# Kernel tuning notes

Hardware: AMD Instinct MI355X
Metric: run time of the kernel (lower is better)

Reference implementation:

```python
import jax, jax.numpy as jnp
import numpy as np

B, T, D_MODEL, N_HEADS = 2, 2048, 1024, 16


def setup_inputs() -> dict:
    key = jax.random.key(0)
    ks = jax.random.split(key, 5)
    w_scale = 0.02
    return {
        "x": jax.random.normal(ks[0], (B, T, D_MODEL), jnp.float32),
        "Wq": jax.random.normal(ks[1], (D_MODEL, D_MODEL), jnp.float32) * w_scale,
        "Wk": jax.random.normal(ks[2], (D_MODEL, D_MODEL), jnp.float32) * w_scale,
        "Wv": jax.random.normal(ks[3], (D_MODEL, D_MODEL), jnp.float32) * w_scale,
        "Wo": jax.random.normal(ks[4], (D_MODEL, D_MODEL), jnp.float32) * w_scale,
    }


def reference(x, Wq, Wk, Wv, Wo):
    Bv, Tv, _ = x.shape
    H = N_HEADS
    D = D_MODEL // H
    # Projections (torch nn.Linear: y = x @ W.T), split heads -> (B, H, T, D)
    q = (x @ Wq.T).reshape(Bv, Tv, H, D).transpose(0, 2, 1, 3)
    k = (x @ Wk.T).reshape(Bv, Tv, H, D).transpose(0, 2, 1, 3)
    v = (x @ Wv.T).reshape(Bv, Tv, H, D).transpose(0, 2, 1, 3)

    scale = jnp.sqrt(jnp.asarray(D, jnp.float32))
    scores = jnp.einsum("bhqd,bhkd->bhqk", q, k) / scale  # (B, H, T, T)

    # ALiBi bias: -|i-j| * slope_h, future positions masked to -inf (causal)
    slopes = jnp.asarray(
        [2.0 ** (-8.0 * h / H) for h in range(1, H + 1)], jnp.float32
    )
    pos = jnp.arange(Tv)
    dist = jnp.abs(pos[None, :] - pos[:, None]).astype(jnp.float32)  # (T, T)
    bias = -dist[None, :, :] * slopes[:, None, None]                 # (H, T, T)
    causal_mask = jnp.triu(jnp.ones((Tv, Tv), dtype=bool), 1)
    bias = jnp.where(causal_mask[None, :, :], -jnp.inf, bias)
    scores = scores + bias[None]  # (B, H, T, T)

    attn = jax.nn.softmax(scores, axis=-1)
    out = jnp.einsum("bhqk,bhkd->bhqd", attn, v)
    out = out.transpose(0, 2, 1, 3).reshape(Bv, Tv, D_MODEL)
    return out @ Wo.T
```

## Files before the change

kernel.cpp:

```cpp
#include <hip/hip_runtime.h>


#define DEV __device__ __forceinline__

typedef __attribute__((ext_vector_type(8))) short short8;
typedef __attribute__((ext_vector_type(4))) float f32x4;
typedef __attribute__((ext_vector_type(4))) unsigned short ushort4v;

DEV unsigned short f2bf(float f) {
  unsigned u = __builtin_bit_cast(unsigned, f);
  u += 0x7fffu + ((u >> 16) & 1u);
  return (unsigned short)(u >> 16);
}
DEV float bf2f(unsigned short u) {
  unsigned x = ((unsigned)u) << 16;
  return __builtin_bit_cast(float, x);
}

DEV void gl2lds16(const void* g, void* l) {
  __builtin_amdgcn_global_load_lds(
      (const __attribute__((address_space(1))) void*)g,
      (__attribute__((address_space(3))) void*)l, 16, 0, 0);
}

__global__ __launch_bounds__(256) void cvt_all(
    const float* __restrict__ x, const float* __restrict__ wq,
    const float* __restrict__ wk, const float* __restrict__ wv,
    const float* __restrict__ wo, unsigned short* __restrict__ xb,
    unsigned short* __restrict__ wqb, unsigned short* __restrict__ wkb,
    unsigned short* __restrict__ wvb, unsigned short* __restrict__ wob) {
  int b = blockIdx.x;
  const float* s;
  unsigned short* d;
  int off;
  if (b < 4096)      { s = x;  d = xb;  off = b; }
  else if (b < 5120) { s = wq; d = wqb; off = b - 4096; }
  else if (b < 6144) { s = wk; d = wkb; off = b - 5120; }
  else if (b < 7168) { s = wv; d = wvb; off = b - 6144; }
  else               { s = wo; d = wob; off = b - 7168; }
  int i = (off * 256 + threadIdx.x) * 4;
  float4 v = *(const float4*)(s + i);
  ushort4v o = {f2bf(v.x), f2bf(v.y), f2bf(v.z), f2bf(v.w)};
  *(ushort4v*)(d + i) = o;
}

__global__ __launch_bounds__(256, 2) void gemm_qkv(
    const unsigned short* __restrict__ A, const unsigned short* __restrict__ Wq,
    const unsigned short* __restrict__ Wk, const unsigned short* __restrict__ Wv,
    unsigned short* __restrict__ Qo, unsigned short* __restrict__ Ko,
    unsigned short* __restrict__ Vo) {
  constexpr int K = 1024;
  __shared__ alignas(16) unsigned short Sm[18432];
  unsigned short* Al = Sm;
  unsigned short* Bl = Sm + 4096;
  const int t = threadIdx.x;
  const int l = t & 63, l15 = l & 15, l4 = l >> 4;
  const int wm = ((t >> 6) & 1) * 64, wn = (t >> 7) * 64;
  const int wsel = blockIdx.x >> 3;
  const int n0 = (blockIdx.x & 7) * 128;
  const int m0 = blockIdx.y * 128;
  const unsigned short* Bm = (wsel == 0) ? Wq : ((wsel == 1) ? Wk : Wv);

  f32x4 zero4 = {0.f, 0.f, 0.f, 0.f};
  f32x4 acc[4][4];
#pragma unroll
  for (int i = 0; i < 4; i++)
#pragma unroll
    for (int j = 0; j < 4; j++) acc[i][j] = zero4;

  const int row0 = t >> 2, seg = (t & 3) * 8;
  const unsigned short* Ag0 = A + (m0 + row0) * K + seg;
  const unsigned short* Ag1 = A + (m0 + row0 + 64) * K + seg;
  const unsigned short* Bg0 = Bm + (n0 + row0) * K + seg;
  const unsigned short* Bg1 = Bm + (n0 + row0 + 64) * K + seg;

  for (int k0 = 0; k0 < K; k0 += 32) {
    gl2lds16(Ag0 + k0, &Al[t * 8]);
    gl2lds16(Ag1 + k0, &Al[2048 + t * 8]);
    gl2lds16(Bg0 + k0, &Bl[t * 8]);
    gl2lds16(Bg1 + k0, &Bl[2048 + t * 8]);
    __syncthreads();
    short8 af[4], bf8[4];
#pragma unroll
    for (int mi = 0; mi < 4; mi++)
      af[mi] = *(const short8*)&Al[(wm + mi * 16 + l15) * 32 + l4 * 8];
#pragma unroll
    for (int ni = 0; ni < 4; ni++)
      bf8[ni] = *(const short8*)&Bl[(wn + ni * 16 + l15) * 32 + l4 * 8];
#pragma unroll
    for (int mi = 0; mi < 4; mi++)
#pragma unroll
      for (int ni = 0; ni < 4; ni++)
        acc[mi][ni] = __builtin_amdgcn_mfma_f32_16x16x32_bf16(
            af[mi], bf8[ni], acc[mi][ni], 0, 0, 0);
    __syncthreads();
  }

  if (wsel != 2) {
    unsigned short* D = (wsel == 0) ? Qo : Ko;
    const float scale = (wsel == 0) ? 0.18033688011112042f : 1.0f;
#pragma unroll
    for (int mi = 0; mi < 4; mi++)
#pragma unroll
      for (int r = 0; r < 4; r++) {
        int m = m0 + wm + mi * 16 + l4 * 4 + r;
        int b = m >> 11, tt = m & 2047;
#pragma unroll
        for (int ni = 0; ni < 4; ni++) {
          int n = n0 + wn + ni * 16 + l15;
          int z = b * 16 + (n >> 6), d = n & 63;
          D[(z * 2048 + tt) * 64 + d] = f2bf(acc[mi][ni][r] * scale);
        }
      }
  } else {
    unsigned short* Tr = Sm + (t >> 6) * 4608;
#pragma unroll
    for (int mi = 0; mi < 4; mi++)
#pragma unroll
      for (int r = 0; r < 4; r++) {
        int tl = mi * 16 + l4 * 4 + r;
#pragma unroll
        for (int ni = 0; ni < 4; ni++)
          Tr[(ni * 16 + l15) * 72 + tl] = f2bf(acc[mi][ni][r]);
      }
    __syncthreads();
    const int bb = m0 >> 11, tbase = m0 & 2047;
#pragma unroll
    for (int it2 = 0; it2 < 8; it2++) {
      int idx = it2 * 256 + t;
      int row = idx >> 4, c = idx & 15;
      int zh = row >> 6, dd = row & 63;
      int wsrc = zh * 2 + (c >> 3);
      short8 v = *(const short8*)&Sm[wsrc * 4608 + dd * 72 + (c & 7) * 8];
      int zg = bb * 16 + (n0 >> 6) + zh;
      *(short8*)&Vo[(zg * 64 + dd) * 2048 + tbase + c * 8] = v;
    }
  }
}

__global__ __launch_bounds__(256, 2) void gemm_o(
    const unsigned short* __restrict__ A, const unsigned short* __restrict__ Bm,
    float* __restrict__ C) {
  constexpr int K = 1024;
  __shared__ alignas(16) unsigned short Al[128 * 32];
  __shared__ alignas(16) unsigned short Bl[64 * 32];
  const int t = threadIdx.x;
  const int l = t & 63, l15 = l & 15, l4 = l >> 4;
  const int wm = ((t >> 6) & 1) * 64, wn = (t >> 7) * 32;
  const int m0 = blockIdx.y * 128, n0 = blockIdx.x * 64;

  f32x4 zero4 = {0.f, 0.f, 0.f, 0.f};
  f32x4 acc[4][2];
#pragma unroll
  for (int i = 0; i < 4; i++)
#pragma unroll
    for (int j = 0; j < 2; j++) acc[i][j] = zero4;

  const int row0 = t >> 2, seg = (t & 3) * 8;
  const unsigned short* Ag0 = A + (m0 + row0) * K + seg;
  const unsigned short* Ag1 = A + (m0 + row0 + 64) * K + seg;
  const unsigned short* Bg0 = Bm + (n0 + row0) * K + seg;

  for (int k0 = 0; k0 < K; k0 += 32) {
    gl2lds16(Ag0 + k0, &Al[t * 8]);
    gl2lds16(Ag1 + k0, &Al[2048 + t * 8]);
    gl2lds16(Bg0 + k0, &Bl[t * 8]);
    __syncthreads();
    short8 af[4], bf2[2];
#pragma unroll
    for (int mi = 0; mi < 4; mi++)
      af[mi] = *(const short8*)&Al[(wm + mi * 16 + l15) * 32 + l4 * 8];
#pragma unroll
    for (int ni = 0; ni < 2; ni++)
      bf2[ni] = *(const short8*)&Bl[(wn + ni * 16 + l15) * 32 + l4 * 8];
#pragma unroll
    for (int mi = 0; mi < 4; mi++)
#pragma unroll
      for (int ni = 0; ni < 2; ni++)
        acc[mi][ni] = __builtin_amdgcn_mfma_f32_16x16x32_bf16(
            af[mi], bf2[ni], acc[mi][ni], 0, 0, 0);
    __syncthreads();
  }
#pragma unroll
  for (int mi = 0; mi < 4; mi++)
#pragma unroll
    for (int r = 0; r < 4; r++) {
      int m = m0 + wm + mi * 16 + l4 * 4 + r;
      float* cp = C + m * 1024 + n0 + wn + l15;
      cp[0] = acc[mi][0][r];
      cp[16] = acc[mi][1][r];
    }
}

__global__ __launch_bounds__(256, 3) void flash_alibi(
    const unsigned short* __restrict__ Q, const unsigned short* __restrict__ Kb,
    const unsigned short* __restrict__ Vt, unsigned short* __restrict__ O0,
    unsigned short* __restrict__ O1, float* __restrict__ L0,
    float* __restrict__ L1) {
  __shared__ alignas(16) unsigned short Kl[2 * 4096];
  __shared__ alignas(16) unsigned short Vl[2 * 4096];
  __shared__ alignas(16) unsigned short Pl[4 * 2304];
  const int t = threadIdx.x, w = t >> 6, l = t & 63, l15 = l & 15, l4 = l >> 4;
  const int g = blockIdx.x;
  const int qt = 15 - (g >> 6);
  const int z = (g & 63) >> 1, s = g & 1;
  const int q0 = qt * 128, h = z & 15;
  const float slope2 = exp2f(-0.5f * (float)(h + 1)) * 1.4426950408889634f;
  const int qrow = q0 + w * 32;

  short8 aq[2][2];
#pragma unroll
  for (int mi = 0; mi < 2; mi++)
#pragma unroll
    for (int ks = 0; ks < 2; ks++)
      aq[mi][ks] = *(const short8*)&Q[(z * 2048 + qrow + mi * 16 + l15) * 64 +
                                      ks * 32 + l4 * 8];

  f32x4 binit[2];
#pragma unroll
  for (int mi = 0; mi < 2; mi++)
#pragma unroll
    for (int r = 0; r < 4; r++)
      binit[mi][r] = -(slope2 * (float)(qrow + mi * 16 + l4 * 4 + r) + 10.0f);

  f32x4 zero4 = {0.f, 0.f, 0.f, 0.f};
  f32x4 o[2][4];
  float lsum[2][4];
#pragma unroll
  for (int mi = 0; mi < 2; mi++)
#pragma unroll
    for (int j = 0; j < 4; j++) {
      o[mi][j] = zero4;
      lsum[mi][j] = 0.f;
    }

  const int row0 = t >> 2, seg8 = (t & 3) * 8;
  const int it0 = s ? (qt + 1) : 0;
  const int nt = qt + 1;

#define ISSUE_LOADS(KV0, BUF)                                                \
  {                                                                          \
    unsigned short* Kd = &Kl[(BUF) * 4096];                                  \
    unsigned short* Vd = &Vl[(BUF) * 4096];                                  \
    gl2lds16(&Kb[(z * 2048 + (KV0) + row0) * 64 + seg8], &Kd[t * 8]);        \
    gl2lds16(&Kb[(z * 2048 + (KV0) + row0) * 64 + 32 + seg8],                \
             &Kd[2048 + t * 8]);                                             \
    gl2lds16(&Vt[(z * 64 + row0) * 2048 + (KV0) + seg8], &Vd[t * 8]);        \
    gl2lds16(&Vt[(z * 64 + row0) * 2048 + (KV0) + 32 + seg8],                \
             &Vd[2048 + t * 8]);                                             \
  }

  ISSUE_LOADS(it0 * 64, 0)

  for (int ii = 0; ii < nt; ++ii) {
    __syncthreads();
    const int kv0 = (it0 + ii) * 64;
    if (ii + 1 < nt) ISSUE_LOADS(kv0 + 64, (ii + 1) & 1)
    if (kv0 > qrow + 31) continue;
    const unsigned short* Kc = &Kl[(ii & 1) * 4096];
    const unsigned short* Vc = &Vl[(ii & 1) * 4096];

    f32x4 sc[2][4];
#pragma unroll
    for (int mi = 0; mi < 2; mi++)
#pragma unroll
      for (int ni = 0; ni < 4; ni++) sc[mi][ni] = binit[mi];
#pragma unroll
    for (int ks = 0; ks < 2; ks++) {
      short8 bk[4];
#pragma unroll
      for (int ni = 0; ni < 4; ni++)
        bk[ni] = *(const short8*)&Kc[(ks * 64 + ni * 16 + l15) * 32 + l4 * 8];
#pragma unroll
      for (int mi = 0; mi < 2; mi++)
#pragma unroll
        for (int ni = 0; ni < 4; ni++)
          sc[mi][ni] = __builtin_amdgcn_mfma_f32_16x16x32_bf16(
              aq[mi][ks], bk[ni], sc[mi][ni], 0, 0, 0);
    }

    const bool needMask = (kv0 + 63 > qrow);
    float jf[4];
#pragma unroll
    for (int ni = 0; ni < 4; ni++) jf[ni] = (float)(kv0 + ni * 16 + l15);

#pragma unroll
    for (int mi = 0; mi < 2; mi++)
#pragma unroll
      for (int r = 0; r < 4; r++) {
        float ps[4];
#pragma unroll
        for (int ni = 0; ni < 4; ni++)
          ps[ni] = __builtin_amdgcn_exp2f(fmaf(slope2, jf[ni], sc[mi][ni][r]));
        if (needMask) {
          int qi = qrow + mi * 16 + l4 * 4 + r;
#pragma unroll
          for (int ni = 0; ni < 4; ni++)
            if (kv0 + ni * 16 + l15 > qi) ps[ni] = 0.f;
        }
        lsum[mi][r] += (ps[0] + ps[1]) + (ps[2] + ps[3]);
        int row = mi * 16 + l4 * 4 + r;
        unsigned short* pp = &Pl[w * 2304 + row * 72 + (l15 & 7)];
#pragma unroll
        for (int ni = 0; ni < 4; ni++)
          pp[((ni * 2 + (l15 >> 3)) ^ l4) * 8] = f2bf(ps[ni]);
      }

    asm volatile("s_waitcnt lgkmcnt(0)" ::: "memory");

    const int rsw = (l15 >> 2) & 3;
#pragma unroll
    for (int ks = 0; ks < 2; ks++) {
      short8 pf[2], vf[4];
#pragma unroll
      for (int mi = 0; mi < 2; mi++)
        pf[mi] = *(const short8*)&Pl[w * 2304 + (mi * 16 + l15) * 72 +
                                     ((ks * 4 + l4) ^ rsw) * 8];
#pragma unroll
      for (int nd = 0; nd < 4; nd++)
        vf[nd] = *(const short8*)&Vc[(ks * 64 + nd * 16 + l15) * 32 + l4 * 8];
#pragma unroll
      for (int mi = 0; mi < 2; mi++)
#pragma unroll
        for (int nd = 0; nd < 4; nd++)
          o[mi][nd] = __builtin_amdgcn_mfma_f32_16x16x32_bf16(
              pf[mi], vf[nd], o[mi][nd], 0, 0, 0);
    }
  }
#undef ISSUE_LOADS

  unsigned short* Op = s ? O1 : O0;
  float* Lp = s ? L1 : L0;
#pragma unroll
  for (int mi = 0; mi < 2; mi++)
#pragma unroll
    for (int r = 0; r < 4; r++) {
      float lv = lsum[mi][r];
#pragma unroll
      for (int off = 1; off < 16; off <<= 1) lv += __shfl_xor(lv, off);
      int tg = qrow + mi * 16 + l4 * 4 + r;
      if (l15 == 0) Lp[z * 2048 + tg] = lv;
      unsigned short* op = &Op[(z * 2048 + tg) * 64 + l15];
#pragma unroll
      for (int nd = 0; nd < 4; nd++) op[nd * 16] = f2bf(o[mi][nd][r]);
    }
}

__global__ __launch_bounds__(256) void combine(
    const unsigned short* __restrict__ O0, const unsigned short* __restrict__ O1,
    const float* __restrict__ L0, const float* __restrict__ L1,
    unsigned short* __restrict__ Ob) {
  int idx = (blockIdx.x * 256 + threadIdx.x) * 8;
  int z = idx >> 17, rem = idx & 131071;
  int tt = rem >> 6, d = rem & 63;
  short8 a = *(const short8*)(O0 + idx);
  short8 b = *(const short8*)(O1 + idx);
  float inv = 1.0f / (L0[z * 2048 + tt] + L1[z * 2048 + tt]);
  short8 o;
#pragma unroll
  for (int j = 0; j < 8; j++) {
    float v = (bf2f((unsigned short)a[j]) + bf2f((unsigned short)b[j])) * inv;
    o[j] = (short)f2bf(v);
  }
  int bq = z >> 4, h = z & 15;
  *(short8*)(Ob + (bq * 2048 + tt) * 1024 + h * 64 + d) = o;
}

extern "C" void kernel_launch(void* const* d_in, const int* in_sizes, int n_in,
                              void* d_out, int out_size, void* d_ws,
                              size_t ws_size, hipStream_t stream) {
  const float* x = (const float*)d_in[0];
  const float* Wq = (const float*)d_in[1];
  const float* Wk = (const float*)d_in[2];
  const float* Wv = (const float*)d_in[3];
  const float* Wo = (const float*)d_in[4];

  char* p = (char*)d_ws;
  unsigned short* xb = (unsigned short*)p;  p += 4096 * 1024 * 2;
  unsigned short* wqb = (unsigned short*)p; p += 1024 * 1024 * 2;
  unsigned short* wkb = (unsigned short*)p; p += 1024 * 1024 * 2;
  unsigned short* wvb = (unsigned short*)p; p += 1024 * 1024 * 2;
  unsigned short* wob = (unsigned short*)p; p += 1024 * 1024 * 2;
  unsigned short* Qb = (unsigned short*)p;  p += 32 * 2048 * 64 * 2;
  unsigned short* Kbf = (unsigned short*)p; p += 32 * 2048 * 64 * 2;
  unsigned short* Vtb = (unsigned short*)p; p += 32 * 2048 * 64 * 2;
  unsigned short* O1 = (unsigned short*)p;  p += 32 * 2048 * 64 * 2;
  float* L0 = (float*)p;                    p += 32 * 2048 * 4;
  float* L1 = (float*)p;                    p += 32 * 2048 * 4;
  unsigned short* O0 = xb;
  unsigned short* Ob = Qb;

  cvt_all<<<8192, 256, 0, stream>>>(x, Wq, Wk, Wv, Wo, xb, wqb, wkb, wvb, wob);
  gemm_qkv<<<dim3(24, 32), 256, 0, stream>>>(xb, wqb, wkb, wvb, Qb, Kbf, Vtb);
  flash_alibi<<<1024, 256, 0, stream>>>(Qb, Kbf, Vtb, O0, O1, L0, L1);
  combine<<<2048, 256, 0, stream>>>(O0, O1, L0, L1, Ob);
  gemm_o<<<dim3(16, 32), 256, 0, stream>>>(Ob, wob, (float*)d_out);
}
```

Baseline: 177.0 us.

## Rewrite QKV GEMM with 256x256 tiles, double-buffered swizzled LDS, phased pipeline

The QKV projection GEMM moves from 128x128 tiles with 4 waves and a single LDS buffer to 256x256 tiles with 8 waves, BK=64, and double-buffered LDS using an XOR-swizzled layout. Global-to-LDS loads for the next K-tile are interleaved with MFMA phases, using explicit vmcnt waits, barriers and setprio. This is meant to hide memory latency and avoid LDS bank conflicts. In exchange it uses 128KB of LDS and more accumulator registers, and the grid shrinks to 192 blocks, which may leave CUs idle on a 256-CU part.

```diff
diff --git a/kernel.cpp b/kernel.cpp
--- a/kernel.cpp
+++ b/kernel.cpp
@@ -44,96 +44,180 @@
   *(ushort4v*)(d + i) = o;
 }
 
-__global__ __launch_bounds__(256, 2) void gemm_qkv(
+__global__ __launch_bounds__(512, 2) void gemm_qkv(
     const unsigned short* __restrict__ A, const unsigned short* __restrict__ Wq,
     const unsigned short* __restrict__ Wk, const unsigned short* __restrict__ Wv,
     unsigned short* __restrict__ Qo, unsigned short* __restrict__ Ko,
     unsigned short* __restrict__ Vo) {
   constexpr int K = 1024;
-  __shared__ alignas(16) unsigned short Sm[18432];
-  unsigned short* Al = Sm;
-  unsigned short* Bl = Sm + 4096;
+  __shared__ alignas(16) unsigned short Sm[65536];
   const int t = threadIdx.x;
-  const int l = t & 63, l15 = l & 15, l4 = l >> 4;
-  const int wm = ((t >> 6) & 1) * 64, wn = (t >> 7) * 64;
-  const int wsel = blockIdx.x >> 3;
-  const int n0 = (blockIdx.x & 7) * 128;
-  const int m0 = blockIdx.y * 128;
-  const unsigned short* Bm = (wsel == 0) ? Wq : ((wsel == 1) ? Wk : Wv);
-
-  f32x4 zero4 = {0.f, 0.f, 0.f, 0.f};
-  f32x4 acc[4][4];
-#pragma unroll
-  for (int i = 0; i < 4; i++)
-#pragma unroll
-    for (int j = 0; j < 4; j++) acc[i][j] = zero4;
-
-  const int row0 = t >> 2, seg = (t & 3) * 8;
-  const unsigned short* Ag0 = A + (m0 + row0) * K + seg;
-  const unsigned short* Ag1 = A + (m0 + row0 + 64) * K + seg;
-  const unsigned short* Bg0 = Bm + (n0 + row0) * K + seg;
-  const unsigned short* Bg1 = Bm + (n0 + row0 + 64) * K + seg;
-
-  for (int k0 = 0; k0 < K; k0 += 32) {
-    gl2lds16(Ag0 + k0, &Al[t * 8]);
-    gl2lds16(Ag1 + k0, &Al[2048 + t * 8]);
-    gl2lds16(Bg0 + k0, &Bl[t * 8]);
-    gl2lds16(Bg1 + k0, &Bl[2048 + t * 8]);
-    __syncthreads();
-    short8 af[4], bf8[4];
-#pragma unroll
-    for (int mi = 0; mi < 4; mi++)
-      af[mi] = *(const short8*)&Al[(wm + mi * 16 + l15) * 32 + l4 * 8];
-#pragma unroll
-    for (int ni = 0; ni < 4; ni++)
-      bf8[ni] = *(const short8*)&Bl[(wn + ni * 16 + l15) * 32 + l4 * 8];
-#pragma unroll
-    for (int mi = 0; mi < 4; mi++)
-#pragma unroll
-      for (int ni = 0; ni < 4; ni++)
-        acc[mi][ni] = __builtin_amdgcn_mfma_f32_16x16x32_bf16(
-            af[mi], bf8[ni], acc[mi][ni], 0, 0, 0);
-    __syncthreads();
-  }
+  const int w = t >> 6, l = t & 63, l15 = l & 15, l4 = l >> 4;
+  const int wr = w >> 2, wc = w & 3;
+  const int wsel = blockIdx.x >> 2;
+  const int n0 = (blockIdx.x & 3) * 256;
+  const int m0 = blockIdx.y * 256;
+  const unsigned short* Bmat = (wsel == 0) ? Wq : ((wsel == 1) ? Wk : Wv);
+
+  const int srow = t >> 3;
+  const int sk = ((t & 7) ^ (srow & 7)) * 8;
+
+#define STG_A(T, H)                                                           \
+  {                                                                           \
+    gl2lds16(A + (m0 + (H)*128 + srow) * K + (T)*64 + sk,                     \
+             &Sm[((T)&1) * 16384 + (H)*8192 + t * 8]);                        \
+    gl2lds16(A + (m0 + (H)*128 + 64 + srow) * K + (T)*64 + sk,                \
+             &Sm[((T)&1) * 16384 + (H)*8192 + 4096 + t * 8]);                 \
+  }
+#define STG_B(T, H)                                                           \
+  {                                                                           \
+    gl2lds16(Bmat + (n0 + (H)*128 + srow) * K + (T)*64 + sk,                  \
+             &Sm[32768 + ((T)&1) * 16384 + (H)*8192 + t * 8]);                \
+    gl2lds16(Bmat + (n0 + (H)*128 + 64 + srow) * K + (T)*64 + sk,             \
+             &Sm[32768 + ((T)&1) * 16384 + (H)*8192 + 4096 + t * 8]);         \
+  }
+
+  f32x4 acc[8][4];
+  {
+    f32x4 z4 = {0.f, 0.f, 0.f, 0.f};
+#pragma unroll
+    for (int i = 0; i < 8; i++)
+#pragma unroll
+      for (int j = 0; j < 4; j++) acc[i][j] = z4;
+  }
+  short8 af[4][2], bf[2][2][2];
+
+#define RD_AF(TT, QM)                                                         \
+  {                                                                           \
+    const unsigned short* Ab_ = &Sm[((TT)&1) * 16384];                        \
+    _Pragma("unroll") for (int mi_ = 0; mi_ < 4; mi_++) {                     \
+      _Pragma("unroll") for (int kk_ = 0; kk_ < 2; kk_++) {                   \
+        af[mi_][kk_] = *(const short8*)&Ab_[                                  \
+            (wr * 128 + (QM)*64 + mi_ * 16 + l15) * 64 +                      \
+            (((kk_ * 4 + l4) ^ (l15 & 7)) * 8)];                              \
+      }                                                                       \
+    }                                                                         \
+  }
+#define RD_BF(TT, QN)                                                         \
+  {                                                                           \
+    const unsigned short* Bb_ = &Sm[32768 + ((TT)&1) * 16384];                \
+    _Pragma("unroll") for (int ni_ = 0; ni_ < 2; ni_++) {                     \
+      _Pragma("unroll") for (int kk_ = 0; kk_ < 2; kk_++) {                   \
+        bf[(QN)][ni_][kk_] = *(const short8*)&Bb_[                            \
+            (wc * 64 + (QN)*32 + ni_ * 16 + l15) * 64 +                       \
+            (((kk_ * 4 + l4) ^ (l15 & 7)) * 8)];                              \
+      }                                                                       \
+    }                                                                         \
+  }
+#define DO_MFMA(QM, QN)                                                       \
+  {                                                                           \
+    _Pragma("unroll") for (int mi_ = 0; mi_ < 4; mi_++) {                     \
+      _Pragma("unroll") for (int ni_ = 0; ni_ < 2; ni_++) {                   \
+        _Pragma("unroll") for (int kk_ = 0; kk_ < 2; kk_++) {                 \
+          acc[(QM)*4 + mi_][(QN)*2 + ni_] =                                   \
+              __builtin_amdgcn_mfma_f32_16x16x32_bf16(                        \
+                  af[mi_][kk_], bf[(QN)][ni_][kk_],                           \
+                  acc[(QM)*4 + mi_][(QN)*2 + ni_], 0, 0, 0);                  \
+        }                                                                     \
+      }                                                                       \
+    }                                                                         \
+  }
+
+#define VMW4 asm volatile("s_waitcnt vmcnt(4)" ::: "memory")
+#define VMW0 asm volatile("s_waitcnt vmcnt(0)" ::: "memory")
+#define NOW ((void)0)
+#define PHASE(RDS, STG, MFMA_, WAIT)                                          \
+  {                                                                           \
+    RDS;                                                                      \
+    STG;                                                                      \
+    __builtin_amdgcn_sched_barrier(0);                                        \
+    __builtin_amdgcn_s_barrier();                                             \
+    __builtin_amdgcn_s_setprio(1);                                            \
+    MFMA_;                                                                    \
+    __builtin_amdgcn_s_setprio(0);                                            \
+    __builtin_amdgcn_sched_barrier(0);                                        \
+    WAIT;                                                                     \
+    __builtin_amdgcn_s_barrier();                                             \
+  }
+
+  STG_B(0, 0); STG_B(0, 1); STG_A(0, 0); STG_A(0, 1);
+  STG_B(1, 0); STG_B(1, 1);
+  VMW4;
+  __builtin_amdgcn_sched_barrier(0);
+  __builtin_amdgcn_s_barrier();
+
+#pragma unroll 1
+  for (int i = 0; i < 7; ++i) {
+    const int TA = 2 * i, TB = TA + 1;
+    PHASE(RD_AF(TA, 0); RD_BF(TA, 0), STG_A(TB, 0),     DO_MFMA(0, 0), NOW);
+    PHASE(RD_BF(TA, 1),               STG_A(TB, 1),     DO_MFMA(0, 1), NOW);
+    PHASE(RD_AF(TA, 1),               STG_B(TA + 2, 0), DO_MFMA(1, 0), NOW);
+    PHASE(NOW,                        STG_B(TA + 2, 1), DO_MFMA(1, 1), VMW4);
+    PHASE(RD_AF(TB, 0); RD_BF(TB, 0), STG_A(TA + 2, 0), DO_MFMA(0, 0), NOW);
+    PHASE(RD_BF(TB, 1),               STG_A(TA + 2, 1), DO_MFMA(0, 1), NOW);
+    PHASE(RD_AF(TB, 1),               STG_B(TB + 2, 0), DO_MFMA(1, 0), NOW);
+    PHASE(NOW,                        STG_B(TB + 2, 1), DO_MFMA(1, 1), VMW4);
+  }
+  PHASE(RD_AF(14, 0); RD_BF(14, 0), STG_A(15, 0), DO_MFMA(0, 0), NOW);
+  PHASE(RD_BF(14, 1),               STG_A(15, 1), DO_MFMA(0, 1), NOW);
+  PHASE(RD_AF(14, 1),               NOW,          DO_MFMA(1, 0), NOW);
+  PHASE(NOW,                        NOW,          DO_MFMA(1, 1), VMW0);
+  PHASE(RD_AF(15, 0); RD_BF(15, 0), NOW,          DO_MFMA(0, 0), NOW);
+  PHASE(RD_BF(15, 1),               NOW,          DO_MFMA(0, 1), NOW);
+  PHASE(RD_AF(15, 1),               NOW,          DO_MFMA(1, 0), NOW);
+  PHASE(NOW,                        NOW,          DO_MFMA(1, 1), NOW);
+
+#undef PHASE
+#undef NOW
+#undef VMW0
+#undef VMW4
+#undef DO_MFMA
+#undef RD_BF
+#undef RD_AF
+#undef STG_B
+#undef STG_A
 
   if (wsel != 2) {
     unsigned short* D = (wsel == 0) ? Qo : Ko;
     const float scale = (wsel == 0) ? 0.18033688011112042f : 1.0f;
-#pragma unroll
-    for (int mi = 0; mi < 4; mi++)
+    const int zb = (n0 >> 6) + wc;
+#pragma unroll
+    for (int mi = 0; mi < 8; mi++)
 #pragma unroll
       for (int r = 0; r < 4; r++) {
-        int m = m0 + wm + mi * 16 + l4 * 4 + r;
+        int m = m0 + wr * 128 + mi * 16 + l4 * 4 + r;
         int b = m >> 11, tt = m & 2047;
-#pragma unroll
-        for (int ni = 0; ni < 4; ni++) {
-          int n = n0 + wn + ni * 16 + l15;
-          int z = b * 16 + (n >> 6), d = n & 63;
-          D[(z * 2048 + tt) * 64 + d] = f2bf(acc[mi][ni][r] * scale);
-        }
+        int z = b * 16 + zb;
+#pragma unroll
+        for (int ni = 0; ni < 4; ni++)
+          D[(z * 2048 + tt) * 64 + ni * 16 + l15] = f2bf(acc[mi][ni][r] * scale);
       }
   } else {
-    unsigned short* Tr = Sm + (t >> 6) * 4608;
-#pragma unroll
-    for (int mi = 0; mi < 4; mi++)
-#pragma unroll
-      for (int r = 0; r < 4; r++) {
-        int tl = mi * 16 + l4 * 4 + r;
-#pragma unroll
-        for (int ni = 0; ni < 4; ni++)
-          Tr[(ni * 16 + l15) * 72 + tl] = f2bf(acc[mi][ni][r]);
+    unsigned short* Tr = Sm + w * 4608;
+    const int b = (m0 + wr * 128) >> 11, tbase = (m0 + wr * 128) & 2047;
+    const int zg = b * 16 + (n0 >> 6) + wc;
+#pragma unroll
+    for (int p = 0; p < 2; p++) {
+#pragma unroll
+      for (int mi = 0; mi < 4; mi++)
+#pragma unroll
+        for (int ni = 0; ni < 4; ni++) {
+          int mg = p * 4 + mi;
+          ushort4v pk = {f2bf(acc[mg][ni][0]), f2bf(acc[mg][ni][1]),
+                         f2bf(acc[mg][ni][2]), f2bf(acc[mg][ni][3])};
+          *(ushort4v*)&Tr[(ni * 16 + l15) * 72 + mi * 16 + l4 * 4] = pk;
+        }
+      asm volatile("s_waitcnt lgkmcnt(0)" ::: "memory");
+      __builtin_amdgcn_sched_barrier(0);
+#pragma unroll
+      for (int j = 0; j < 8; j++) {
+        int idx = j * 64 + l;
+        int d = idx >> 3, c = idx & 7;
+        short8 v = *(const short8*)&Tr[d * 72 + c * 8];
+        *(short8*)&Vo[(zg * 64 + d) * 2048 + tbase + p * 64 + c * 8] = v;
       }
-    __syncthreads();
-    const int bb = m0 >> 11, tbase = m0 & 2047;
-#pragma unroll
-    for (int it2 = 0; it2 < 8; it2++) {
-      int idx = it2 * 256 + t;
-      int row = idx >> 4, c = idx & 15;
-      int zh = row >> 6, dd = row & 63;
-      int wsrc = zh * 2 + (c >> 3);
-      short8 v = *(const short8*)&Sm[wsrc * 4608 + dd * 72 + (c & 7) * 8];
-      int zg = bb * 16 + (n0 >> 6) + zh;
-      *(short8*)&Vo[(zg * 64 + dd) * 2048 + tbase + c * 8] = v;
+      asm volatile("s_waitcnt lgkmcnt(0)" ::: "memory");
+      __builtin_amdgcn_sched_barrier(0);
     }
   }
 }
@@ -391,7 +475,7 @@
   unsigned short* Ob = Qb;
 
   cvt_all<<<8192, 256, 0, stream>>>(x, Wq, Wk, Wv, Wo, xb, wqb, wkb, wvb, wob);
-  gemm_qkv<<<dim3(24, 32), 256, 0, stream>>>(xb, wqb, wkb, wvb, Qb, Kbf, Vtb);
+  gemm_qkv<<<dim3(12, 16), 512, 0, stream>>>(xb, wqb, wkb, wvb, Qb, Kbf, Vtb);
   flash_alibi<<<1024, 256, 0, stream>>>(Qb, Kbf, Vtb, O0, O1, L0, L1);
   combine<<<2048, 256, 0, stream>>>(O0, O1, L0, L1, Ob);
   gemm_o<<<dim3(16, 32), 256, 0, stream>>>(Ob, wob, (float*)d_out);
```

New measurement: 176.3 us. No clear change (-0.4%).
